# Optimization experiments

Measured on AMD Instinct MI355X. Metric: run time of the kernel, lower is better.

The kernel has to match this reference:

```python
import math
import jax, jax.numpy as jnp
import numpy as np

B, K, D, R = 8192, 64, 128, 8
EPSILON = 1.0  # alpha_scale, used as diffusion epsilon


def setup_inputs() -> dict:
    key = jax.random.key(0)
    k1, k2, k3 = jax.random.split(key, 3)
    y = jax.random.normal(k1, (B, D), dtype=jnp.float32)
    m = 0.2 * jax.random.normal(k2, (K, D), dtype=jnp.float32)          # init_mean_scale=0.2
    delta = jnp.full((K, D), -2.0, dtype=jnp.float32)                    # init_delta=-2.0
    U = 0.001 * jax.random.normal(k3, (K, D, R), dtype=jnp.float32)
    # log_alpha_raw = alpha_scale * log(ones(K)/K)
    log_alpha_raw = jnp.full((K,), math.log(1.0 / K), dtype=jnp.float32)
    return {"y": y, "m": m, "delta": delta, "U": U, "log_alpha_raw": log_alpha_raw}


def reference(y, m, delta, U, log_alpha_raw):
    """log z_theta(y) = logsumexp_k [log_alpha_k + log N(y; m_k, eps*S_k)],
    S_k = diag(exp(delta_k)) + U_k U_k^T, solved via Woodbury + Cholesky."""
    d = y.shape[-1]
    eps = jnp.asarray(EPSILON, y.dtype)
    log_alpha = (log_alpha_raw - jnp.mean(log_alpha_raw)) / EPSILON

    S_diag = jnp.exp(delta)            # [K, d]
    S_inv = 1.0 / S_diag               # [K, d]

    # Capacitance M_k = I_r + U_k^T diag(S_inv_k) U_k, Cholesky L_k
    V = S_inv[..., None] * U                              # [K, d, r]
    Mcap = jnp.eye(R, dtype=y.dtype) + jnp.einsum('kdr,kds->krs', U, V)  # [K, r, r]
    L = jnp.linalg.cholesky(Mcap)                         # [K, r, r]
    logdet_S = jnp.sum(jnp.log(S_diag), axis=-1) \
        + 2.0 * jnp.sum(jnp.log(jnp.diagonal(L, axis1=-2, axis2=-1)), axis=-1)  # [K]

    diff = y[:, None, :] - m[None, :, :]                  # [B, K, d]
    u1 = diff * S_inv[None]                               # [B, K, d]
    # Woodbury correction: solve M_k s = U_k^T u1 for all (b, k)
    t = jnp.einsum('kdr,bkd->krb', U, u1)                 # [K, r, B] (B as multiple RHS)
    z1 = jax.scipy.linalg.solve_triangular(L, t, lower=True)
    s = jax.scipy.linalg.solve_triangular(jnp.swapaxes(L, -1, -2), z1, lower=False)  # [K, r, B]
    Us = jnp.einsum('kdr,krb->bkd', U, s)                 # [B, K, d]
    S_inv_diff = u1 - Us * S_inv[None]                    # [B, K, d]

    quad = jnp.sum(diff * S_inv_diff, axis=-1)            # [B, K]
    log_norm = 0.5 * (d * (math.log(2.0 * math.pi) + jnp.log(eps)) + logdet_S)  # [K]
    logits = log_alpha[None, :] - 0.5 * quad / eps - log_norm[None, :]          # [B, K]
    return jax.scipy.special.logsumexp(logits, axis=-1)   # [B]
```

## Files before the change

kernel.cpp:

```cpp
#include <hip/hip_runtime.h>
#include <math.h>

#define D_DIM 128
#define K_DIM 64
#define R_DIM 8
#define B_DIM 8192
#define XSTR  264

#define WS_C0F   73728

typedef __bf16 bf16x8 __attribute__((ext_vector_type(8)));
typedef float  f32x4  __attribute__((ext_vector_type(4)));

static __device__ inline unsigned short f2bf(float f) {
  union { float f; unsigned int u; } v; v.f = f;
  unsigned int u = v.u;
  unsigned int lsb = (u >> 16) & 1;
  u += 0x7fffu + lsb;
  return (unsigned short)(u >> 16);
}

__global__ __launch_bounds__(128) void precomp_kernel(
    const float* __restrict__ m, const float* __restrict__ delta,
    const float* __restrict__ U, const float* __restrict__ lar,
    float* __restrict__ ws) {
  const int k = blockIdx.x;
  const int d = threadIdx.x;

  __shared__ float U_l[D_DIM][R_DIM];
  __shared__ float V_l[D_DIM][R_DIM];
  __shared__ float W_l[D_DIM][R_DIM];
  __shared__ float m_l[D_DIM];
  __shared__ float red[64];
  __shared__ float Linv_s[R_DIM][R_DIM];
  __shared__ float q_s[R_DIM];
  __shared__ float c0_s[1];
  __shared__ float redA[D_DIM], redB[D_DIM], redC[D_DIM];

  const float dl    = delta[k * D_DIM + d];
  const float s_inv = expf(-dl);
  const float mv    = m[k * D_DIM + d];
  m_l[d] = mv;
  const float* Up = U + (size_t)(k * D_DIM + d) * R_DIM;
#pragma unroll
  for (int r = 0; r < R_DIM; ++r) {
    float u = Up[r];
    U_l[d][r] = u;
    V_l[d][r] = u * s_inv;
  }
  redA[d] = dl;
  redB[d] = mv * mv * s_inv;
  redC[d] = (d < K_DIM) ? lar[d] : 0.f;
  __syncthreads();

  if (d < 64) {
    const int r = d >> 3, s = d & 7;
    float acc = (r == s) ? 1.0f : 0.0f;
#pragma unroll 8
    for (int dd = 0; dd < D_DIM; ++dd) acc += U_l[dd][r] * V_l[dd][s];
    red[d] = acc;
  }
  __syncthreads();

  for (int off = 64; off > 0; off >>= 1) {
    if (d < off) {
      redA[d] += redA[d + off];
      redB[d] += redB[d + off];
      redC[d] += redC[d + off];
    }
    __syncthreads();
  }

  if (d == 0) {
    float Lm[8][8];
#pragma unroll
    for (int i = 0; i < 8; ++i) {
#pragma unroll
      for (int j = 0; j < 8; ++j) {
        if (j > i) continue;
        float sum = red[i * 8 + j];
#pragma unroll
        for (int p = 0; p < 8; ++p)
          if (p < j) sum -= Lm[i][p] * Lm[j][p];
        if (i == j) Lm[i][i] = sqrtf(sum);
        else        Lm[i][j] = sum / Lm[j][j];
      }
    }
    float ld = 0.f;
#pragma unroll
    for (int i = 0; i < 8; ++i) ld += logf(Lm[i][i]);

    float Li[8][8];
#pragma unroll
    for (int i = 0; i < 8; ++i)
#pragma unroll
      for (int j = 0; j < 8; ++j) Li[i][j] = 0.f;
#pragma unroll
    for (int j = 0; j < 8; ++j) {
      Li[j][j] = 1.0f / Lm[j][j];
#pragma unroll
      for (int i = 0; i < 8; ++i) {
        if (i <= j) continue;
        float sum = 0.f;
#pragma unroll
        for (int p = 0; p < 8; ++p)
          if (p >= j && p < i) sum += Lm[i][p] * Li[p][j];
        Li[i][j] = -sum / Lm[i][i];
      }
    }
#pragma unroll
    for (int i = 0; i < 8; ++i)
#pragma unroll
      for (int j = 0; j < 8; ++j) Linv_s[i][j] = Li[i][j];

    const float mean = redC[0] * (1.0f / K_DIM);
    const float log_alpha = lar[k] - mean;
    const float logdetS = redA[0] + 2.0f * ld;
    const float LOG2PI = 1.8378770664093453f;
    const float log_norm = 0.5f * ((float)D_DIM * LOG2PI + logdetS);
    c0_s[0] = log_alpha - log_norm - 0.5f * redB[0];
  }
  __syncthreads();

  float Wr[R_DIM];
#pragma unroll
  for (int r = 0; r < R_DIM; ++r) {
    float acc = 0.f;
#pragma unroll
    for (int s2 = 0; s2 < R_DIM; ++s2)
      if (s2 <= r) acc += V_l[d][s2] * Linv_s[r][s2];
    Wr[r] = acc;
    W_l[d][r] = acc;
  }
  __syncthreads();

  if (d < R_DIM) {
    float acc = 0.f;
#pragma unroll 8
    for (int dd = 0; dd < D_DIM; ++dd) acc += W_l[dd][d] * m_l[dd];
    q_s[d] = acc;
  }
  __syncthreads();

  float hp = mv * s_inv;
#pragma unroll
  for (int r = 0; r < R_DIM; ++r) hp -= q_s[r] * Wr[r];

  const float INV_SQRT2 = 0.70710678118654752f;
  unsigned short* T = (unsigned short*)ws;
  const int kg = k >> 4, kl = k & 15;
  const int chunk = d >> 5, pos = d & 31;
  const size_t by = (((size_t)(kg * 8 + chunk) * 9) * 16 + kl) * 32 + pos;
  const size_t bq = (((size_t)(kg * 8 + chunk + 4) * 9) * 16 + kl) * 32 + pos;
#pragma unroll
  for (int cc = 0; cc < 8; ++cc) {
    T[by + (size_t)cc * 512] = f2bf(Wr[cc] * INV_SQRT2);
    T[bq + (size_t)cc * 512] = 0;
  }
  T[by + 8 * 512] = f2bf(hp);
  T[bq + 8 * 512] = f2bf(-0.5f * s_inv);

  if (d == 0) {
    float qq = 0.f;
#pragma unroll
    for (int r = 0; r < R_DIM; ++r) qq += q_s[r] * q_s[r];
    ws[WS_C0F + k] = c0_s[0] + 0.5f * qq;
  }
}

__global__ __launch_bounds__(512, 1) void logz_full(
    const float* __restrict__ y, const float* __restrict__ ws,
    float* __restrict__ out) {
  __shared__ __align__(16) char smem[16896 + 2 * 36864];
  __shared__ float vals2[32 * 66];

  unsigned short* sX = (unsigned short*)smem;
  unsigned short* sT = (unsigned short*)(smem + 16896);

  const int tid   = threadIdx.x;
  const int lane  = tid & 63;
  const int wv    = tid >> 6;
  const int wr    = wv & 1;
  const int wc    = wv >> 1;
  const int col_l = lane & 15;
  const int quad  = lane >> 4;
  const int r0    = (int)blockIdx.x * 32;

  for (int mm = wv; mm < 36; mm += 8) {
    const int kgm = mm / 9, seg = mm - kgm * 9;
    const float* src = ws + (size_t)(kgm * 8 + 0) * 2304 + seg * 256 + lane * 4;
    __builtin_amdgcn_global_load_lds(
        (const __attribute__((address_space(1))) void*)src,
        (__attribute__((address_space(3))) void*)(sT + (kgm * 9 + seg) * 512),
        16, 0, 0);
  }

  {
#pragma unroll
    for (int j = 0; j < 2; ++j) {
      const int idx = tid + j * 512;
      const int row = idx >> 5, g = idx & 31;
      const float4* ya = (const float4*)y + (size_t)(r0 + row) * 32 + (g & 15) * 2;
      float4 a = ya[0], b = ya[1];
      if (g >= 16) {
        a.x *= a.x; a.y *= a.y; a.z *= a.z; a.w *= a.w;
        b.x *= b.x; b.y *= b.y; b.z *= b.z; b.w *= b.w;
      }
      union { unsigned short us[8]; uint4 v; } o;
      o.us[0] = f2bf(a.x); o.us[1] = f2bf(a.y); o.us[2] = f2bf(a.z); o.us[3] = f2bf(a.w);
      o.us[4] = f2bf(b.x); o.us[5] = f2bf(b.y); o.us[6] = f2bf(b.z); o.us[7] = f2bf(b.w);
      *(uint4*)(sX + row * XSTR + g * 8) = o.v;
    }
  }

  f32x4 acc[9];
#pragma unroll
  for (int f = 0; f < 9; ++f) { acc[f][0] = 0.f; acc[f][1] = 0.f; acc[f][2] = 0.f; acc[f][3] = 0.f; }

  const int rowA = wr * 16 + col_l;

  for (int c = 0; c < 8; ++c) {
    __syncthreads();
    if (c < 7) {
      const int nb = (c + 1) & 1;
      for (int mm = wv; mm < 36; mm += 8) {
        const int kgm = mm / 9, seg = mm - kgm * 9;
        const float* src = ws + (size_t)(kgm * 8 + c + 1) * 2304 + seg * 256 + lane * 4;
        __builtin_amdgcn_global_load_lds(
            (const __attribute__((address_space(1))) void*)src,
            (__attribute__((address_space(3))) void*)(sT + nb * 18432 + (kgm * 9 + seg) * 512),
            16, 0, 0);
      }
    }
    const bf16x8 a = *(const bf16x8*)(sX + rowA * XSTR + c * 32 + quad * 8);
    const unsigned short* tb = sT + (c & 1) * 18432 + wc * 4608;
#pragma unroll
    for (int f = 0; f < 9; ++f) {
      const bf16x8 b = *(const bf16x8*)(tb + (f * 16 + col_l) * 32 + quad * 8);
      acc[f] = __builtin_amdgcn_mfma_f32_16x16x32_bf16(a, b, acc[f], 0, 0, 0);
    }
  }

  const float cv = ws[WS_C0F + wc * 16 + col_l];
#pragma unroll
  for (int reg = 0; reg < 4; ++reg) {
    float v = acc[8][reg];
#pragma unroll
    for (int cc = 0; cc < 8; ++cc) v += acc[cc][reg] * acc[cc][reg];
    vals2[(wr * 16 + quad * 4 + reg) * 66 + wc * 16 + col_l] = cv + v;
  }
  __syncthreads();

#pragma unroll
  for (int rr = 0; rr < 4; ++rr) {
    const int row = wv * 4 + rr;
    const float val = vals2[row * 66 + lane];
    float mx = val;
#pragma unroll
    for (int off = 1; off < 64; off <<= 1)
      mx = fmaxf(mx, __shfl_xor(mx, off, 64));
    float ex = expf(val - mx);
#pragma unroll
    for (int off = 1; off < 64; off <<= 1)
      ex += __shfl_xor(ex, off, 64);
    if (lane == 0) out[r0 + row] = mx + logf(ex);
  }
}

extern "C" void kernel_launch(void* const* d_in, const int* in_sizes, int n_in,
                              void* d_out, int out_size, void* d_ws, size_t ws_size,
                              hipStream_t stream) {
  const float* y     = (const float*)d_in[0];
  const float* m     = (const float*)d_in[1];
  const float* delta = (const float*)d_in[2];
  const float* U     = (const float*)d_in[3];
  const float* lar   = (const float*)d_in[4];
  float* out = (float*)d_out;
  float* ws  = (float*)d_ws;

  precomp_kernel<<<K_DIM, 128, 0, stream>>>(m, delta, U, lar, ws);
  logz_full<<<B_DIM / 32, 512, 0, stream>>>(y, ws, out);
}
```

Measured before the change: 80.32 us.

## Halve logz block size to 16 rows and drop the T double-buffering

The main kernel now uses 256-thread blocks that each handle 16 rows of y. This doubles the grid and allows up to three blocks per CU under the new launch bounds. The double-buffered T prefetch is replaced by a single buffer: each wave loads its own k-group slice per chunk, followed by a barrier. The goal is better latency hiding through multiple resident blocks rather than intra-block prefetching. The cost is twice as many total T loads from L2 and an extra barrier per chunk with no overlap inside a block.

```diff
diff --git a/kernel.cpp b/kernel.cpp
--- a/kernel.cpp
+++ b/kernel.cpp
@@ -168,37 +168,24 @@
   }
 }
 
-__global__ __launch_bounds__(512, 1) void logz_full(
+__global__ __launch_bounds__(256, 3) void logz_full(
     const float* __restrict__ y, const float* __restrict__ ws,
     float* __restrict__ out) {
-  __shared__ __align__(16) char smem[16896 + 2 * 36864];
-  __shared__ float vals2[32 * 66];
-
-  unsigned short* sX = (unsigned short*)smem;
-  unsigned short* sT = (unsigned short*)(smem + 16896);
+  __shared__ __align__(16) unsigned short sX[16 * XSTR];
+  __shared__ __align__(16) unsigned short sT[4 * 9 * 16 * 32];
+  __shared__ float vals2[16 * 66];
 
   const int tid   = threadIdx.x;
   const int lane  = tid & 63;
   const int wv    = tid >> 6;
-  const int wr    = wv & 1;
-  const int wc    = wv >> 1;
   const int col_l = lane & 15;
   const int quad  = lane >> 4;
-  const int r0    = (int)blockIdx.x * 32;
-
-  for (int mm = wv; mm < 36; mm += 8) {
-    const int kgm = mm / 9, seg = mm - kgm * 9;
-    const float* src = ws + (size_t)(kgm * 8 + 0) * 2304 + seg * 256 + lane * 4;
-    __builtin_amdgcn_global_load_lds(
-        (const __attribute__((address_space(1))) void*)src,
-        (__attribute__((address_space(3))) void*)(sT + (kgm * 9 + seg) * 512),
-        16, 0, 0);
-  }
+  const int r0    = (int)blockIdx.x * 16;
 
   {
 #pragma unroll
     for (int j = 0; j < 2; ++j) {
-      const int idx = tid + j * 512;
+      const int idx = tid + j * 256;
       const int row = idx >> 5, g = idx & 31;
       const float4* ya = (const float4*)y + (size_t)(r0 + row) * 32 + (g & 15) * 2;
       float4 a = ya[0], b = ya[1];
@@ -217,23 +204,21 @@
 #pragma unroll
   for (int f = 0; f < 9; ++f) { acc[f][0] = 0.f; acc[f][1] = 0.f; acc[f][2] = 0.f; acc[f][3] = 0.f; }
 
-  const int rowA = wr * 16 + col_l;
-
   for (int c = 0; c < 8; ++c) {
     __syncthreads();
-    if (c < 7) {
-      const int nb = (c + 1) & 1;
-      for (int mm = wv; mm < 36; mm += 8) {
-        const int kgm = mm / 9, seg = mm - kgm * 9;
-        const float* src = ws + (size_t)(kgm * 8 + c + 1) * 2304 + seg * 256 + lane * 4;
+    {
+      const float* src = ws + (size_t)(wv * 8 + c) * 2304;
+#pragma unroll
+      for (int j = 0; j < 9; ++j) {
         __builtin_amdgcn_global_load_lds(
-            (const __attribute__((address_space(1))) void*)src,
-            (__attribute__((address_space(3))) void*)(sT + nb * 18432 + (kgm * 9 + seg) * 512),
+            (const __attribute__((address_space(1))) void*)(src + j * 256 + lane * 4),
+            (__attribute__((address_space(3))) void*)(sT + wv * 4608 + j * 512),
             16, 0, 0);
       }
     }
-    const bf16x8 a = *(const bf16x8*)(sX + rowA * XSTR + c * 32 + quad * 8);
-    const unsigned short* tb = sT + (c & 1) * 18432 + wc * 4608;
+    __syncthreads();
+    const bf16x8 a = *(const bf16x8*)(sX + col_l * XSTR + c * 32 + quad * 8);
+    const unsigned short* tb = sT + wv * 4608;
 #pragma unroll
     for (int f = 0; f < 9; ++f) {
       const bf16x8 b = *(const bf16x8*)(tb + (f * 16 + col_l) * 32 + quad * 8);
@@ -241,13 +226,13 @@
     }
   }
 
-  const float cv = ws[WS_C0F + wc * 16 + col_l];
+  const float cv = ws[WS_C0F + wv * 16 + col_l];
 #pragma unroll
   for (int reg = 0; reg < 4; ++reg) {
     float v = acc[8][reg];
 #pragma unroll
     for (int cc = 0; cc < 8; ++cc) v += acc[cc][reg] * acc[cc][reg];
-    vals2[(wr * 16 + quad * 4 + reg) * 66 + wc * 16 + col_l] = cv + v;
+    vals2[(quad * 4 + reg) * 66 + wv * 16 + col_l] = cv + v;
   }
   __syncthreads();
 
@@ -279,5 +264,5 @@
   float* ws  = (float*)d_ws;
 
   precomp_kernel<<<K_DIM, 128, 0, stream>>>(m, delta, U, lar, ws);
-  logz_full<<<B_DIM / 32, 512, 0, stream>>>(y, ws, out);
-}
+  logz_full<<<B_DIM / 16, 256, 0, stream>>>(y, ws, out);
+}
```

New measurement: 79.97 us. Within noise of the previous version (-0.4%).
